# Kernel optimization log

Measured on AMD Instinct MI355X. Metric: run time of the kernel, lower is better.

## Reference

```python
import jax, jax.numpy as jnp
import numpy as np

SQ3, SQ5, SQ15 = 3.0**0.5, 5.0**0.5, 15.0**0.5
M0, M1, M2 = 128, 64, 32
DIM = M0 + 3*M1 + 5*M2  # 480
N_GRAPHS, ATOMS_PER, N_BLOCKS = 512, 16, 8
N_NODES = N_GRAPHS * ATOMS_PER
N_EDGES = 100000
CUTOFF = 5.0
AVG_DEGREE = 15.57
AVG_NUM_NODES = 18.03
ATOM_MAP = np.array([-1, 0, -1, -1, -1, -1, 1, 2, 3, 4], dtype=np.int32)


def _sph(u):
    # component-normalized real spherical harmonics l=1,2 of unit vectors u [E,3]
    x, y, z = u[:, 0], u[:, 1], u[:, 2]
    sh1 = SQ3 * u
    sh2 = jnp.stack([SQ15*x*y, SQ15*y*z, 0.5*SQ5*(3.0*z*z - 1.0),
                     SQ15*x*z, 0.5*SQ15*(x*x - y*y)], axis=-1)
    return sh1, sh2


def _seg_softmax(logits, seg, n):
    m = jax.ops.segment_max(logits, seg, num_segments=n)
    e = jnp.exp(logits - m[seg])
    s = jax.ops.segment_sum(e, seg, num_segments=n)
    return e / (s[seg] + 1e-9)


def _energy(pos, fp, node_atom, edge_src, edge_dst, batch):
    (atom_table, rbf_centers, rbf_width, deg_W1, deg_W2, deg_W3,
     blk_Wv0, blk_Wv1, blk_Wv2, blk_Ws0, blk_Ws1, blk_Ws2,
     blk_rW1, blk_rW2, blk_rW3, blk_Wa_src, blk_Wa_dst, blk_Wa_e, blk_wa,
     blk_ff1, blk_ff2, blk_fg1, blk_fg2, blk_fW1, blk_fW2,
     ln_g, ln_b, head_W0, head_out) = fp
    N = pos.shape[0]
    mapped = jnp.asarray(ATOM_MAP)[node_atom]
    f0 = atom_table[mapped]                       # [N,128] scalar channels
    f1 = jnp.zeros((N, M1, 3), f0.dtype)
    f2 = jnp.zeros((N, M2, 5), f0.dtype)

    vec = pos[edge_src] - pos[edge_dst]           # [E,3]
    r = jnp.sqrt(jnp.sum(vec*vec, axis=1) + 1e-12)
    u = vec / r[:, None]
    sh1, sh2 = _sph(u)
    rbf = jnp.exp(-0.5 * ((r[:, None] - rbf_centers[None, :]) / rbf_width[None, :])**2)  # [E,128]

    # edge-degree embedding: radial-weighted SH scattered to dst, scaled by avg degree
    h = jax.nn.silu(rbf @ deg_W1)
    h = jax.nn.silu(h @ deg_W2)
    g = h @ deg_W3                                 # [E,224]
    g0, g1, g2 = g[:, :M0], g[:, M0:M0+M1], g[:, M0+M1:]
    inv = 1.0 / (AVG_DEGREE ** 0.5)
    f0 = f0 + inv * jax.ops.segment_sum(g0, edge_dst, num_segments=N)
    f1 = f1 + inv * jax.ops.segment_sum(g1[:, :, None]*sh1[:, None, :], edge_dst, num_segments=N)
    f2 = f2 + inv * jax.ops.segment_sum(g2[:, :, None]*sh2[:, None, :], edge_dst, num_segments=N)

    for i in range(N_BLOCKS):
        s0, s1, s2 = f0[edge_src], f1[edge_src], f2[edge_src]
        h = jax.nn.silu(rbf @ blk_rW1[i])
        h = jax.nn.silu(h @ blk_rW2[i])
        g = h @ blk_rW3[i]
        g0, g1, g2 = g[:, :M0], g[:, M0:M0+M1], g[:, M0+M1:]
        # equivariant tensor-product messages: value path (radial-gated) + SH-injection path
        m0 = (s0 @ blk_Wv0[i]) * g0 + s0 @ blk_Ws0[i]
        m1 = jnp.einsum('ecx,cd->edx', s1, blk_Wv1[i]) * g1[:, :, None] \
             + (s0 @ blk_Ws1[i])[:, :, None] * sh1[:, None, :]
        m2 = jnp.einsum('ecx,cd->edx', s2, blk_Wv2[i]) * g2[:, :, None] \
             + (s0 @ blk_Ws2[i])[:, :, None] * sh2[:, None, :]
        # scalar attention, softmax over incoming edges per destination node
        z = jnp.tanh(s0 @ blk_Wa_src[i] + f0[edge_dst] @ blk_Wa_dst[i] + h @ blk_Wa_e[i])
        a = _seg_softmax(z @ blk_wa[i], edge_dst, N)  # [E]
        f0 = f0 + jax.ops.segment_sum(a[:, None]*m0, edge_dst, num_segments=N)
        f1 = f1 + jax.ops.segment_sum(a[:, None, None]*m1, edge_dst, num_segments=N)
        f2 = f2 + jax.ops.segment_sum(a[:, None, None]*m2, edge_dst, num_segments=N)
        # equivariant FFN: scalar MLP + scalar-gated per-l channel mixing
        f0 = f0 + jax.nn.silu(f0 @ blk_ff1[i]) @ blk_ff2[i]
        f1 = f1 + jnp.einsum('ncx,cd->ndx', f1, blk_fW1[i]) * jax.nn.sigmoid(f0 @ blk_fg1[i])[:, :, None]
        f2 = f2 + jnp.einsum('ncx,cd->ndx', f2, blk_fW2[i]) * jax.nn.sigmoid(f0 @ blk_fg2[i])[:, :, None]

    flat = jnp.concatenate([f0, f1.reshape(N, 3*M1), f2.reshape(N, 5*M2)], axis=1)  # [N,480]
    mu = jnp.mean(flat, axis=1, keepdims=True)
    var = jnp.var(flat, axis=1, keepdims=True)
    flat = (flat - mu) * jax.lax.rsqrt(var + 1e-5) * ln_g + ln_b
    # head: only the 0e part can reach the final 1x0e output (equivariance)
    e_node = jax.nn.silu(flat[:, :M0] @ head_W0) @ head_out  # [N,1]
    energy = jax.ops.segment_sum(e_node[:, 0], batch, num_segments=N_GRAPHS) / (AVG_NUM_NODES ** 0.5)
    return energy  # [B]


def setup_inputs() -> dict:
    key = jax.random.key(0)
    rng = np.random.default_rng(0)
    B, A = N_GRAPHS, ATOMS_PER
    pos_np = rng.uniform(0.0, 6.0, size=(B, A, 3)).astype(np.float32)
    d = np.linalg.norm(pos_np[:, :, None, :] - pos_np[:, None, :, :], axis=-1)
    mask = (d < CUTOFF) & (d > 1e-6)
    gi, si, di = np.nonzero(mask)
    src = np.resize((gi*A + si).astype(np.int32), N_EDGES)
    dst = np.resize((gi*A + di).astype(np.int32), N_EDGES)
    atoms = rng.choice(np.array([1, 6, 7, 8, 9], dtype=np.int32), size=B*A)
    batch = np.repeat(np.arange(B, dtype=np.int32), A)

    ks = iter(jax.random.split(key, 40))
    def W(shape, fan):
        return jax.random.normal(next(ks), shape, jnp.float32) / np.sqrt(fan)
    D3 = M0 + M1 + M2  # 224
    return dict(
        pos=jnp.asarray(pos_np.reshape(B*A, 3)),
        atom_table=W((5, M0), 1.0),
        rbf_centers=jnp.linspace(0.0, CUTOFF, 128),
        rbf_width=jnp.full((128,), 0.25, jnp.float32),
        deg_W1=W((128, 64), 128), deg_W2=W((64, 64), 64), deg_W3=W((64, D3), 64),
        blk_Wv0=W((8, M0, M0), M0), blk_Wv1=W((8, M1, M1), M1), blk_Wv2=W((8, M2, M2), M2),
        blk_Ws0=W((8, M0, M0), M0), blk_Ws1=W((8, M0, M1), M0), blk_Ws2=W((8, M0, M2), M0),
        blk_rW1=W((8, 128, 64), 128), blk_rW2=W((8, 64, 64), 64), blk_rW3=W((8, 64, D3), 64),
        blk_Wa_src=W((8, M0, 32), M0), blk_Wa_dst=W((8, M0, 32), M0), blk_Wa_e=W((8, 64, 32), 64),
        blk_wa=W((8, 32), 32),
        blk_ff1=W((8, M0, 4*M0), M0), blk_ff2=W((8, 4*M0, M0), 4*M0),
        blk_fg1=W((8, M0, M1), M0), blk_fg2=W((8, M0, M2), M0),
        blk_fW1=W((8, M1, M1), M1), blk_fW2=W((8, M2, M2), M2),
        ln_g=jnp.ones((DIM,), jnp.float32), ln_b=jnp.zeros((DIM,), jnp.float32),
        head_W0=W((M0, M0), M0), head_out=W((M0, 1), M0),
        node_atom=jnp.asarray(atoms), edge_src=jnp.asarray(src),
        edge_dst=jnp.asarray(dst), batch=jnp.asarray(batch),
    )


def reference(pos, atom_table, rbf_centers, rbf_width, deg_W1, deg_W2, deg_W3,
              blk_Wv0, blk_Wv1, blk_Wv2, blk_Ws0, blk_Ws1, blk_Ws2,
              blk_rW1, blk_rW2, blk_rW3, blk_Wa_src, blk_Wa_dst, blk_Wa_e, blk_wa,
              blk_ff1, blk_ff2, blk_fg1, blk_fg2, blk_fW1, blk_fW2,
              ln_g, ln_b, head_W0, head_out,
              node_atom, edge_src, edge_dst, batch):
    fp = (atom_table, rbf_centers, rbf_width, deg_W1, deg_W2, deg_W3,
          blk_Wv0, blk_Wv1, blk_Wv2, blk_Ws0, blk_Ws1, blk_Ws2,
          blk_rW1, blk_rW2, blk_rW3, blk_Wa_src, blk_Wa_dst, blk_Wa_e, blk_wa,
          blk_ff1, blk_ff2, blk_fg1, blk_fg2, blk_fW1, blk_fW2,
          ln_g, ln_b, head_W0, head_out)

    def _tot(p):
        e = _energy(p, fp, node_atom, edge_src, edge_dst, batch)
        return jnp.sum(e), e

    (_, energy), gpos = jax.value_and_grad(_tot, has_aux=True)(pos)
    forces = -gpos  # dy = -dE/dpos, as in the torch autograd.grad call
    return energy, forces
```

## Files before the change

### kernel.cpp

```cpp
#include <hip/hip_runtime.h>
#include <string.h>
#include <math.h>

#define NE 100000
#define NN 8192
#define NG 512
#define CHF 25000
#define NF 4
#define CHB 20000
#define NB 5
#define CHIF 50000
#define NIF 2
#define CHIB 34000
#define NIB 3
#define NNC 8192

#define SQ3F  1.7320508075688772f
#define SQ5F  2.23606797749979f
#define SQ15F 3.872983346207417f

__constant__ int c_amap[10] = {-1,0,-1,-1,-1,-1,1,2,3,4};

typedef __attribute__((ext_vector_type(4))) float f32x4;
typedef __attribute__((ext_vector_type(8))) short bf16x8;
// ... 352 lines not shown
__global__ void k_geom(const float* __restrict__ pos, const int* __restrict__ src, const int* __restrict__ dst,
                       float* __restrict__ U, float* __restrict__ Rr, float* __restrict__ SH2b){
  int e = blockIdx.x*256 + threadIdx.x;
  if (e >= NE) return;
  int s = src[e], d = dst[e];
  float vx = pos[s*3+0]-pos[d*3+0];
  float vy = pos[s*3+1]-pos[d*3+1];
  float vz = pos[s*3+2]-pos[d*3+2];
  float r = sqrtf(vx*vx+vy*vy+vz*vz + 1e-12f);
  float ux=vx/r, uy=vy/r, uz=vz/r;
  U[e*3+0]=ux; U[e*3+1]=uy; U[e*3+2]=uz;
  Rr[e]=r;
  SH2b[e*5+0]=SQ15F*ux*uy;
  SH2b[e*5+1]=SQ15F*uy*uz;
  SH2b[e*5+2]=0.5f*SQ5F*(3.0f*uz*uz-1.0f);
  SH2b[e*5+3]=SQ15F*ux*uz;
  SH2b[e*5+4]=0.5f*SQ15F*(ux*ux-uy*uy);
}

__global__ void k_f0init(const int* __restrict__ na, const float* __restrict__ at, float* __restrict__ f0){
  int t = blockIdx.x*256 + threadIdx.x;
  if (t >= NN*128) return;
  int n = t>>7, j = t&127;
  int m = c_amap[na[n]];
  f0[t] = at[m*128+j];
}

__global__ void k_postblk(const float* __restrict__ x0,const float* __restrict__ x1,const float* __restrict__ x2,
                          float* __restrict__ y0,float* __restrict__ y1,float* __restrict__ y2,
                          const float* __restrict__ S, unsigned short* __restrict__ ck,
                          const float* __restrict__ Pl, const int* __restrict__ dst, float* __restrict__ AB){
  int t = blockIdx.x*256 + threadIdx.x;
  if (t < NE) AB[t] = Pl[t]/(S[dst[t]]+1e-9f);
  if (t >= NN*480) return;
  float v;
  if (t < NN*128){ int n=t>>7; v = x0[t] + y0[t]/(S[n]+1e-9f); y0[t]=v; }
  else if (t < NN*320){ int q=t-NN*128; int n=q/192; v = x1[q] + y1[q]/(S[n]+1e-9f); y1[q]=v; }
  else { int q=t-NN*320; int n=q/160; v = x2[q] + y2[q]/(S[n]+1e-9f); y2[q]=v; }
  ck[t] = f2b(v);
}

__global__ void k_q3(const float* __restrict__ f0,const float* __restrict__ f1,const float* __restrict__ f2,
                     unsigned short* __restrict__ ck){
  int t = blockIdx.x*256 + threadIdx.x;
  if (t >= NN*480) return;
  float v;
  if (t < NN*128) v = f0[t];
  else if (t < NN*320) v = f1[t-NN*128];
  else v = f2[t-NN*320];
  ck[t] = f2b(v);
}
__global__ void k_dq3x2(const unsigned short* __restrict__ cka, const unsigned short* __restrict__ ckb,
                        float* __restrict__ a0,float* __restrict__ a1,float* __restrict__ a2,
                        float* __restrict__ b0,float* __restrict__ b1,float* __restrict__ b2){
  int t = blockIdx.x*256 + threadIdx.x;
  if (t >= NN*480) return;
  float va = b2f(cka[t]), vb = b2f(ckb[t]);
  if (t < NN*128){ a0[t]=va; b0[t]=vb; }
  else if (t < NN*320){ int q=t-NN*128; a1[q]=va; b1[q]=vb; }
  else { int q=t-NN*320; a2[q]=va; b2[q]=vb; }
}

template<bool INIT>
__global__ __launch_bounds__(512) void k_agg(
  float* __restrict__ f0o,float* __restrict__ f1o,float* __restrict__ f2o,
  const float* __restrict__ SC,const float* __restrict__ sv1,const float* __restrict__ sv2,
  const float* __restrict__ g,const float* __restrict__ U,const float* __restrict__ SH2b,
  const float* __restrict__ aArr,const int* __restrict__ keys,const int* __restrict__ dst,
  float* __restrict__ SACC, int c0, int c1)
{
  __shared__ float acc[7680];
  int b = blockIdx.x, lo = b<<4;
  int e0 = lbound(keys, NE, lo), e1 = lbound(keys, NE, lo+16);
  if (e0 < c0) e0 = c0;
  if (e1 > c1) e1 = c1;
  if (e0 >= e1) return;
  for (int i=threadIdx.x;i<7680;i+=512) acc[i]=0.0f;
  __syncthreads();
  const int j = threadIdx.x;
  const float inv = 1.0f/sqrtf(15.57f);
  int cat=3, cc_=0, xx_=0;
  if (j<128){ cat=0; }
  else if (j<320){ cat=1; int t=j-128; cc_=t/3; xx_=t-3*cc_; }
  else if (j<480){ cat=2; int t=j-320; cc_=t/5; xx_=t-5*cc_; }
  float sacc=0.0f;
  for (int e=e0; e<e1; ++e){
    int el = e - c0;
    float a = INIT ? inv : aArr[e];
    int nl = dst[e]&15;
    if (cat==0){
      float m = INIT ? g[el*224+j] : (SC[(size_t)el*352+j]*g[el*224+j] + SC[(size_t)el*352+128+j]);
      acc[nl*480+j] += a*m;
    } else if (cat==1){
      int t=j-128;
      float sh = SQ3F*U[e*3+xx_];
      float m = INIT ? g[el*224+128+cc_]*sh : (sv1[el*192+t]*g[el*224+128+cc_] + SC[(size_t)el*352+256+cc_]*sh);
      acc[nl*480+j] += a*m;
    } else if (cat==2){
      int t=j-320;
      float sh = SH2b[e*5+xx_];
      float m = INIT ? g[el*224+192+cc_]*sh : (sv2[el*160+t]*g[el*224+192+cc_] + SC[(size_t)el*352+320+cc_]*sh);
      acc[nl*480+j] += a*m;
    } else if (!INIT && j<496){
      if (nl==(j-480)) sacc += a;
    }
  }
  __syncthreads();
  for (int i=threadIdx.x;i<7680;i+=512){
    int nl=i/480, jj=i-480*nl, n=lo+nl;
    float v=acc[i];
    if (jj<128) f0o[n*128+jj]+=v;
    else if (jj<320) f1o[n*192+jj-128]+=v;
    else f2o[n*160+jj-320]+=v;
  }
  if (!INIT && j>=480 && j<496) SACC[lo+(j-480)] += sacc;
}

__global__ __launch_bounds__(640) void k_scat(
  float* __restrict__ df0, float* __restrict__ df1, float* __restrict__ df2,
  const float* __restrict__ DE0, const float* __restrict__ DZD,
  const float* __restrict__ DE1, const float* __restrict__ DE2,
  const int* __restrict__ src, const int* __restrict__ dst, int c0, int c1)
{
  __shared__ float acc[7680];
  int b=blockIdx.x, lo=b<<4;
  int e0=lbound(dst,NE,lo), e1=lbound(dst,NE,lo+16);
  if (e0 < c0) e0 = c0;
  if (e1 > c1) e1 = c1;
  for (int i=threadIdx.x;i<7680;i+=640) acc[i]=0.0f;
  __syncthreads();
  const int j=threadIdx.x;
  for (int e=e0;e<e1;++e){
    int el=e-c0;
    int sl=(src[e]&15)*480, dl=(dst[e]&15)*480;
    if (j<128) acc[sl+j] += DE0[el*128+j];
    else if (j<256){ int q=j-128; acc[dl+q] += DZD[el*128+q]; }
    else if (j<448){ int q=j-256; acc[sl+128+q] += DE1[el*192+q]; }
    else if (j<608){ int q=j-448; acc[sl+320+q] += DE2[el*160+q]; }
    __syncthreads();
  }
  for (int i=threadIdx.x;i<7680;i+=640){
    int nl=i/480, jj=i-480*nl, n=lo+nl;
    float v=acc[i];
    if (jj<128) df0[n*128+jj]+=v;
    else if (jj<320) df1[n*192+jj-128]+=v;
    else df2[n*160+jj-320]+=v;
  }
}

__global__ __launch_bounds__(256) void k_ssum(
  const float* __restrict__ FA0,const float* __restrict__ FA1,const float* __restrict__ FA2,
  const float* __restrict__ FB0,const float* __restrict__ FB1,const float* __restrict__ FB2,
  const float* __restrict__ DY0,const float* __restrict__ DY1,const float* __restrict__ DY2,
  float* __restrict__ SSUM)
{
  int n=blockIdx.x*4+(threadIdx.x>>6), lane=threadIdx.x&63;
  if (n>=NN) return;
  float s=0.0f;
  for (int j=lane;j<480;j+=64){
    float d,g;
    if (j<128){ d=FB0[n*128+j]-FA0[n*128+j]; g=DY0[n*128+j]; }
    else if (j<320){ int q=j-128; d=FB1[n*192+q]-FA1[n*192+q]; g=DY1[n*192+q]; }
    else { int q=j-320; d=FB2[n*160+q]-FA2[n*160+q]; g=DY2[n*160+q]; }
    s += d*g;
  }
  s = wred64(s);
  if (lane==0) SSUM[n]=s;
}

__global__ __launch_bounds__(256) void k_bedge(
  float* __restrict__ SC, float* __restrict__ SV1, float* __restrict__ SV2,
  const float* __restrict__ g, const float* __restrict__ U, const float* __restrict__ SH2b,
  const float* __restrict__ df0,const float* __restrict__ df1,const float* __restrict__ df2,
  const int* __restrict__ dst, const float* __restrict__ SSUM, const float* __restrict__ wa,
  float* __restrict__ Z, const float* __restrict__ aArr,
  float* __restrict__ DG, float* __restrict__ DSH1, float* __restrict__ DSH2,
  int c0, int cnt)
{
  int w=threadIdx.x>>6, lane=threadIdx.x&63;
  int el=blockIdx.x*4+w;
  if (el>=cnt) return;
  int e=c0+el;
  int d=dst[e];
  float s=0.0f;
  for (int j=lane;j<480;j+=64){
    float m, dfv;
    if (j<128){
      m = SC[(size_t)el*352+j]*g[el*224+j] + SC[(size_t)el*352+128+j];
      dfv = df0[(size_t)d*128+j];
    } else if (j<320){
      int t=j-128, c=t/3, x=t-3*c;
      m = SV1[el*192+t]*g[el*224+128+c] + SC[(size_t)el*352+256+c]*(SQ3F*U[e*3+x]);
      dfv = df1[(size_t)d*192+t];
    } else {
      int t=j-320, c=t/5, x=t-5*c;
      m = SV2[el*160+t]*g[el*224+192+c] + SC[(size_t)el*352+320+c]*SH2b[e*5+x];
      dfv = df2[(size_t)d*160+t];
    }
    s += m*dfv;
  }
  s = wred64(s);
  s = __shfl(s,0,64);
  float a = aArr[e];
  float dlam = a*(s - SSUM[d]);
  if (lane<32){
    float z = Z[(size_t)el*32+lane];
    Z[(size_t)el*32+lane] = dlam*wa[lane]*(1.0f-z*z);
  }
  {
    float* row = SC + (size_t)el*352;
    for (int j=lane;j<128;j+=64){
      float dm = a*df0[(size_t)d*128+j];
      float sv = row[j];
      row[128+j] = dm;
      row[j] = dm*g[el*224+j];
      DG[el*224+j] = dm*sv;
    }
  }
  {
    float dm0=a*df1[(size_t)d*192+lane*3+0];
    float dm1=a*df1[(size_t)d*192+lane*3+1];
    float dm2=a*df1[(size_t)d*192+lane*3+2];
    float sw1o=SC[(size_t)el*352+256+lane];
    float g1=g[el*224+128+lane];
    float c0v=dm0*sw1o, c1v=dm1*sw1o, c2v=dm2*sw1o;
    c0v=wred64(c0v); c1v=wred64(c1v); c2v=wred64(c2v);
    if (lane==0){ DSH1[e*3+0]+=c0v; DSH1[e*3+1]+=c1v; DSH1[e*3+2]+=c2v; }
    float sh0=SQ3F*U[e*3+0], sh1=SQ3F*U[e*3+1], sh2=SQ3F*U[e*3+2];
    SC[(size_t)el*352+256+lane]=dm0*sh0+dm1*sh1+dm2*sh2;
    float sv0o=SV1[el*192+lane*3+0], sv1o=SV1[el*192+lane*3+1], sv2o=SV1[el*192+lane*3+2];
    DG[el*224+128+lane]=dm0*sv0o+dm1*sv1o+dm2*sv2o;
    SV1[el*192+lane*3+0]=dm0*g1; SV1[el*192+lane*3+1]=dm1*g1; SV1[el*192+lane*3+2]=dm2*g1;
  }
  {
    float dm[5]={0,0,0,0,0}, svo[5]={0,0,0,0,0};
    float sw2o=0.0f, g2=0.0f;
    if (lane<32){
      #pragma unroll
      for (int x=0;x<5;x++){ dm[x]=a*df2[(size_t)d*160+lane*5+x]; svo[x]=SV2[el*160+lane*5+x]; }
      sw2o=SC[(size_t)el*352+320+lane]; g2=g[el*224+192+lane];
    }
    float c[5];
    #pragma unroll
    for (int x=0;x<5;x++){ c[x]=dm[x]*sw2o; c[x]=wred64(c[x]); }
    if (lane==0){
      #pragma unroll
      for (int x=0;x<5;x++) DSH2[e*5+x]+=c[x];
    }
    if (lane<32){
      float dsw=0.0f, dg2=0.0f;
      #pragma unroll
      for (int x=0;x<5;x++){ dsw+=dm[x]*SH2b[e*5+x]; dg2+=dm[x]*svo[x]; }
      SC[(size_t)el*352+320+lane]=dsw;
      DG[el*224+192+lane]=dg2;
      #pragma unroll
      for (int x=0;x<5;x++) SV2[el*160+lane*5+x]=dm[x]*g2;
    }
  }
}

template<int CD,int X>
__global__ void k_gateback(const float* __restrict__ dfB, float* __restrict__ V,
                           const float* __restrict__ P12, float* __restrict__ DPa, int poff){
  int t=blockIdx.x*256+threadIdx.x;
  if (t>=NN*CD) return;
  int n=t/CD, d=t-n*CD;
  float p=P12[(size_t)n*96+poff+d];
  float dp=0.0f;
  #pragma unroll
  for (int x=0;x<X;x++){ dp += dfB[(size_t)t*X+x]*V[(size_t)t*X+x]; }
  #pragma unroll
  for (int x=0;x<X;x++){ V[(size_t)t*X+x] = dfB[(size_t)t*X+x]*p; }
  DPa[(size_t)n*96+poff+d] = dp*p*(1.0f-p);
}

__global__ __launch_bounds__(256) void k_dr(const float* __restrict__ DRBF, const float* __restrict__ Rr,
    const float* __restrict__ cen, const float* __restrict__ wid, float* __restrict__ DRa, int c0, int cnt){
  int w=threadIdx.x>>6, lane=threadIdx.x&63;
  int el=blockIdx.x*4+w;
  if (el>=cnt) return;
  int e=c0+el;
  float r=Rr[e], s=0.0f;
  for (int k=lane;k<128;k+=64){
    float c=cen[k], wd=wid[k];
    float t=(r-c)/wd;
    float rb=expf(-0.5f*t*t);
    s += DRBF[el*128+k]*rb*((c-r)/(wd*wd));
  }
  s=wred64(s);
  if (lane==0) DRa[e]+=s;
}

__global__ __launch_bounds__(256) void k_initback(
  const float* __restrict__ df0,const float* __restrict__ df1,const float* __restrict__ df2,
  const int* __restrict__ dst,
  const float* __restrict__ g,const float* __restrict__ U,const float* __restrict__ SH2b,
  float* __restrict__ DG,float* __restrict__ DSH1,float* __restrict__ DSH2, int c0, int cnt)
{
  int w=threadIdx.x>>6, lane=threadIdx.x&63;
  int el=blockIdx.x*4+w;
  if (el>=cnt) return;
  int e=c0+el;
  int d=dst[e];
  const float inv=1.0f/sqrtf(15.57f);
  for (int j=lane;j<128;j+=64) DG[el*224+j]=inv*df0[d*128+j];
  float sh0=SQ3F*U[e*3+0], sh1=SQ3F*U[e*3+1], sh2=SQ3F*U[e*3+2];
  float df10=df1[d*192+lane*3+0], df11=df1[d*192+lane*3+1], df12=df1[d*192+lane*3+2];
  float g1=g[el*224+128+lane];
  DG[el*224+128+lane]=inv*(df10*sh0+df11*sh1+df12*sh2);
  float c0v=g1*df10, c1v=g1*df11, c2v=g1*df12;
  c0v=wred64(c0v); c1v=wred64(c1v); c2v=wred64(c2v);
  if (lane==0){ DSH1[e*3+0]+=inv*c0v; DSH1[e*3+1]+=inv*c1v; DSH1[e*3+2]+=inv*c2v; }
  float cc[5]={0,0,0,0,0};
  if (lane<32){
    float g2=g[el*224+192+lane];
    float dgv=0.0f;
    #pragma unroll
    for (int x=0;x<5;x++){ float dfv=df2[d*160+lane*5+x]; dgv+=dfv*SH2b[e*5+x]; cc[x]=g2*dfv; }
    DG[el*224+192+lane]=inv*dgv;
  }
  #pragma unroll
  for (int x=0;x<5;x++) cc[x]=wred64(cc[x]);
  if (lane==0){
    #pragma unroll
    for (int x=0;x<5;x++) DSH2[e*5+x]+=inv*cc[x];
  }
}

__global__ void k_geoback(const float* __restrict__ DRa, const float* __restrict__ DSH1, const float* __restrict__ DSH2,
                          const float* __restrict__ U, const float* __restrict__ Rr,
                          const int* __restrict__ src, const int* __restrict__ dst,
                          float* __restrict__ DPOS){
  int e=blockIdx.x*256+threadIdx.x;
  if (e>=NE) return;
  float ux=U[e*3+0], uy=U[e*3+1], uz=U[e*3+2];
  float r=Rr[e];
  float dux=SQ3F*DSH1[e*3+0], duy=SQ3F*DSH1[e*3+1], duz=SQ3F*DSH1[e*3+2];
  float d0=DSH2[e*5+0],d1=DSH2[e*5+1],d2=DSH2[e*5+2],d3=DSH2[e*5+3],d4=DSH2[e*5+4];
  dux += SQ15F*(uy*d0+uz*d3+ux*d4);
  duy += SQ15F*(ux*d0+uz*d1-uy*d4);
  duz += SQ15F*(uy*d1+ux*d3)+3.0f*SQ5F*uz*d2;
  float dr=DRa[e];
  float dot=dux*ux+duy*uy+duz*uz;
  float dvx=(dux-dot*ux)/r+dr*ux;
  float dvy=(duy-dot*uy)/r+dr*uy;
  float dvz=(duz-dot*uz)/r+dr*uz;
  int s=src[e], d=dst[e];
  atomicAdd(&DPOS[s*3+0],dvx); atomicAdd(&DPOS[s*3+1],dvy); atomicAdd(&DPOS[s*3+2],dvz);
  atomicAdd(&DPOS[d*3+0],-dvx); atomicAdd(&DPOS[d*3+1],-dvy); atomicAdd(&DPOS[d*3+2],-dvz);
}

__global__ void k_forces(const float* __restrict__ DPOS, float* __restrict__ o){
  int i=blockIdx.x*256+threadIdx.x;
  if (i<NN*3) o[i]=-DPOS[i];
}

__global__ __launch_bounds__(64) void k_lnhead(
  const float* __restrict__ f0,const float* __restrict__ f1,const float* __restrict__ f2,
  const float* __restrict__ lng,const float* __restrict__ lnb,
  const float* __restrict__ W0,const float* __restrict__ hout,
  float* __restrict__ EN, float* __restrict__ df0,float* __restrict__ df1,float* __restrict__ df2)
{
  __shared__ float xh[480];
  __shared__ float fl[128];
  __shared__ float dyv[128];
  __shared__ float dxh[128];
  int n=blockIdx.x, lane=threadIdx.x;
  const float c0=1.0f/sqrtf(18.03f);
  for (int i=lane;i<480;i+=64){
    float v=(i<128)? f0[n*128+i] : (i<320)? f1[n*192+(i-128)] : f2[n*160+(i-320)];
    xh[i]=v;
  }
  __syncthreads();
  float s1=0.0f,s2=0.0f;
  for (int i=lane;i<480;i+=64){ float v=xh[i]; s1+=v; s2+=v*v; }
  s1=wred64(s1); s2=wred64(s2);
  float mu=__shfl(s1,0,64)*(1.0f/480.0f);
  float var=__shfl(s2,0,64)*(1.0f/480.0f)-mu*mu;
  float rstd=rsqrtf(var+1e-5f);
  for (int i=lane;i<480;i+=64) xh[i]=(xh[i]-mu)*rstd;
  __syncthreads();
  for (int k=lane;k<128;k+=64) fl[k]=xh[k]*lng[k]+lnb[k];
  __syncthreads();
  float y0=0.0f,y1=0.0f;
  for (int k=0;k<128;k++){ float f=fl[k]; y0+=f*W0[k*128+lane]; y1+=f*W0[k*128+lane+64]; }
  float e = siluf(y0)*hout[lane] + siluf(y1)*hout[lane+64];
  e=wred64(e);
  if (lane==0) EN[n]=e*c0;
  dyv[lane]=c0*hout[lane]*dsiluf(y0);
  dyv[lane+64]=c0*hout[lane+64]*dsiluf(y1);
  __syncthreads();
  float d0=0.0f,d1=0.0f;
  for (int j=0;j<128;j++){ float dv=dyv[j]; d0+=dv*W0[lane*128+j]; d1+=dv*W0[(lane+64)*128+j]; }
  dxh[lane]=d0*lng[lane];
  dxh[lane+64]=d1*lng[lane+64];
  __syncthreads();
  float s3=dxh[lane]+dxh[lane+64];
  float s4=dxh[lane]*xh[lane]+dxh[lane+64]*xh[lane+64];
  s3=wred64(s3); s4=wred64(s4);
  float m1=__shfl(s3,0,64)*(1.0f/480.0f);
  float m2=__shfl(s4,0,64)*(1.0f/480.0f);
  for (int i=lane;i<480;i+=64){
    float dv=rstd*(((i<128)?dxh[i]:0.0f)-m1-xh[i]*m2);
    if (i<128) df0[n*128+i]=dv;
    else if (i<320) df1[n*192+(i-128)]=dv;
    else df2[n*160+(i-320)]=dv;
  }
}

__global__ void k_esum(const float* __restrict__ EN, float* __restrict__ out){
  int b=blockIdx.x*64+threadIdx.x;
  if (b<NG){
    float s=0.0f;
    for (int k=0;k<16;k++) s+=EN[b*16+k];
    out[b]=s;
  }
}

#define MG(MT,TB,ACC,ACT,GA,SP,AR,DM,PO, A,IDX,B,C,M,Nd,K, CEN,WID,DMp,POp) \
  k_mgemm<MT,TB,ACC,ACT,GA,SP,AR,DM,PO><<<dim3((unsigned)(((M)+(MT)-1)/(MT)),(unsigned)(((Nd)+63)/64)),dim3(256),0,stream>>>((A),(IDX),(B),(C),(M),(Nd),(K),(CEN),(WID),(DMp),(POp))
#define MGEMM(MT,TB,ACC,ACT,GA, A,IDX,B,C,M,Nd,K) MG(MT,TB,ACC,ACT,GA,false,false,false,false, A,IDX,B,C,M,Nd,K, nullptr,nullptr,nullptr,nullptr)
#define MGEMM3(MT,TB,ACC,ACT,GA, A,IDX,B,C,M,Nd,K) MG(MT,TB,ACC,ACT,GA,true,false,false,false, A,IDX,B,C,M,Nd,K, nullptr,nullptr,nullptr,nullptr)
#define MEINS(CI,CO,X,TB,ACC,GA, A,IDX,Wt,C,M) \
  k_meinsum<CI,CO,X,TB,ACC,GA,false,false><<<dim3((unsigned)(((M)*(X)+63)/64)),dim3(256),0,stream>>>((A),(IDX),(Wt),(C),(M),nullptr,0,0)
#define MEINS3(CI,CO,X,TB,ACC,GA, A,IDX,Wt,C,M) \
  k_meinsum<CI,CO,X,TB,ACC,GA,true,false><<<dim3((unsigned)(((M)*(X)+63)/64)),dim3(256),0,stream>>>((A),(IDX),(Wt),(C),(M),nullptr,0,0)
#define MEINSG(CI,CO,X,SP, A,Wt,C,M, Pp,POFF) \
  k_meinsum<CI,CO,X,false,false,false,SP,true><<<dim3((unsigned)(((M)*(X)+63)/64)),dim3(256),0,stream>>>((A),nullptr,(Wt),(C),(M),(Pp),96,(POFF))
#define G256(n) dim3((unsigned)(((n)+255)/256)),dim3(256),0,stream
#define GW4(n) dim3((unsigned)(((n)+3)/4)),dim3(256),0,stream

extern "C" void kernel_launch(void* const* d_in, const int* in_sizes, int n_in,
                              void* d_out, int out_size, void* d_ws, size_t ws_size,
                              hipStream_t stream)
{
  const float* pos =(const float*)d_in[0];
  const float* atab=(const float*)d_in[1];
  const float* rbfc=(const float*)d_in[2];
  const float* rbfw=(const float*)d_in[3];
  const float* degW1=(const float*)d_in[4];
  const float* degW2=(const float*)d_in[5];
  const float* degW3=(const float*)d_in[6];
  const float* Wv0=(const float*)d_in[7];
  const float* Wv1=(const float*)d_in[8];
  const float* Wv2=(const float*)d_in[9];
  const float* Ws0=(const float*)d_in[10];
  const float* Ws1=(const float*)d_in[11];
  const float* Ws2=(const float*)d_in[12];
  const float* rW1=(const float*)d_in[13];
  const float* rW2=(const float*)d_in[14];
  const float* rW3=(const float*)d_in[15];
  const float* WaS=(const float*)d_in[16];
  const float* WaD=(const float*)d_in[17];
  const float* WaE=(const float*)d_in[18];
  const float* wab=(const float*)d_in[19];
  const float* ff1=(const float*)d_in[20];
  const float* ff2=(const float*)d_in[21];
  const float* fg1=(const float*)d_in[22];
  const float* fg2=(const float*)d_in[23];
  const float* fW1=(const float*)d_in[24];
  const float* fW2=(const float*)d_in[25];
  const float* lng=(const float*)d_in[26];
  const float* lnb=(const float*)d_in[27];
  const float* W0h=(const float*)d_in[28];
  const float* hout=(const float*)d_in[29];
  const int* natom=(const int*)d_in[30];
  const int* esrc=(const int*)d_in[31];
  const int* edst=(const int*)d_in[32];

  float* Wp=(float*)d_ws;
  size_t off=0;
  auto al=[&](size_t n)->float*{ float* q=Wp+off; off+=n; return q; };

  const size_t SLOT = (size_t)NN*480;
  unsigned short* CKB = (unsigned short*)al((9*SLOT+1)/2);
  float* FA0=al((size_t)NN*128); float* FA1=al((size_t)NN*192); float* FA2=al((size_t)NN*160);
  float* FB0=al((size_t)NN*128); float* FB1=al((size_t)NN*192); float* FB2=al((size_t)NN*160);
  float* DI0=al((size_t)NN*128); float* DI1=al((size_t)NN*192); float* DI2=al((size_t)NN*160);
  float* DY0=al((size_t)NN*128); float* DY1=al((size_t)NN*192); float* DY2=al((size_t)NN*160);
  float* U=al((size_t)NE*3); float* Rr=al(NE); float* SH2b=al((size_t)NE*5);
  float* ABLK=al(8ULL*NE); float* LAM=al(NE);
  float* SSUM=al(NN); float* ENODE=al(NN); float* SACC=al(NN);
  float* DRr=al(NE); float* DSH1=al((size_t)NE*3); float* DSH2=al((size_t)NE*5);
  float* DPOS=al((size_t)NN*3);
  float* WCATF=al(8ULL*128*352);
  float* WCATZ=al(8ULL*320*32);
  float* WCATG=al(8ULL*128*96);
  int* ROWS =(int*)al(NN+1);
  int* CNT  =(int*)al(NN);
  int* POSB =(int*)al(NN);
  int* PERMB=(int*)al(NE);
  int* ESRC2=(int*)al(NE);
  int* EDST2=(int*)al(NE);

  const size_t UNI = 28800000;
  float* UN = al(UNI);
  float* TBc=UN;
  float* DTc=TBc+(size_t)NNC*512;
  float* P12=DTc+(size_t)NNC*512;
  float* V1 =P12+(size_t)NN*96;
  float* V2 =V1 +(size_t)NN*192;
  float* DPb=V2 +(size_t)NN*160;
  float* F0N=DPb+(size_t)NN*96;

  float* outE=(float*)d_out;
  float* outF=outE+NG;

  if (off*sizeof(float) > ws_size){
    k_sentinel<<<G256(out_size)>>>(outE, out_size, (float)ws_size);
    return;
  }

  (void)hipMemsetAsync(CNT,0,NN*sizeof(int),stream);
  k_hist<<<G256(NE)>>>(edst,CNT,NE);
  k_scan0<<<dim3(1),dim3(256),0,stream>>>(CNT,ROWS);
  (void)hipMemcpyAsync(POSB,ROWS,NN*sizeof(int),hipMemcpyDeviceToDevice,stream);
  k_fillperm<<<G256(NE)>>>(edst,POSB,PERMB,NE);
  k_mkedge<<<G256(NE)>>>(PERMB,esrc,edst,ESRC2,EDST2);
  k_wcat<<<G256(8*128*352)>>>(Wv0,Ws0,Ws1,Ws2,WCATF);
  k_wcatz<<<G256(8*320*32)>>>(WaS,WaD,WaE,WCATZ);
  k_wcatg<<<G256(8*128*96)>>>(fg1,fg2,WCATG);

  k_geom<<<G256(NE)>>>(pos,ESRC2,EDST2,U,Rr,SH2b);
  k_f0init<<<G256(NN*128)>>>(natom,atab,FA0);
  (void)hipMemsetAsync(FA1,0,(size_t)NN*352*4,stream);
  (void)hipMemsetAsync(DRr,0,(size_t)NE*4,stream);
  (void)hipMemsetAsync(DSH1,0,(size_t)NE*3*4,stream);
  (void)hipMemsetAsync(DSH2,0,(size_t)NE*5*4,stream);
  (void)hipMemsetAsync(DPOS,0,(size_t)NN*3*4,stream);

  {
    float* H1=UN; float* H2=H1+(size_t)CHIF*64; float* Gc=H2+(size_t)CHIF*64;
    for (int cc=0;cc<NIF;cc++){
      int c0e=cc*CHIF, cnt=(c0e+CHIF<=NE)?CHIF:(NE-c0e);
      MG(64,false,false,1,false, true,true,false,false, Rr+c0e,nullptr,degW1,H1, cnt,64,128, rbfc,rbfw,nullptr,nullptr);
      MGEMM3(64,false,false,1,false, H1,nullptr,degW2,H2, cnt,64,64);
      MGEMM3(64,false,false,0,false, H2,nullptr,degW3,Gc, cnt,224,64);
      k_agg<true><<<dim3(NG),dim3(512),0,stream>>>(FA0,FA1,FA2,
        nullptr,nullptr,nullptr, Gc,U,SH2b, nullptr, EDST2,EDST2, nullptr, c0e,c0e+cnt);
    }
  }
  k_q3<<<G256(NN*480)>>>(FA0,FA1,FA2, CKB);

  float *c0_=FA0,*c1_=FA1,*c2_=FA2, *n0_=FB0,*n1_=FB1,*n2_=FB2;

  {
    float* H1  =UN;
    float* H2  =H1  +(size_t)CHF*64;
    float* Gc  =H2  +(size_t)CHF*64;
    float* SCAT=Gc  +(size_t)CHF*224;
    float* SV1 =SCAT+(size_t)CHF*352;
    float* SV2 =SV1 +(size_t)CHF*192;
    float* Zc  =SV2 +(size_t)CHF*160;
    for (int i=0;i<8;i++){
      const float* Wv1i=Wv1+(size_t)i*4096; const float* Wv2i=Wv2+(size_t)i*1024;
      const float* rW1i=rW1+(size_t)i*8192; const float* rW2i=rW2+(size_t)i*4096; const float* rW3i=rW3+(size_t)i*14336;
      const float* WZi=WCATZ+(size_t)i*10240;
      const float* ff1i=ff1+(size_t)i*65536; const float* ff2i=ff2+(size_t)i*65536;
      const float* fgCi=WCATG+(size_t)i*12288;
      const float* fW1i=fW1+(size_t)i*4096; const float* fW2i=fW2+(size_t)i*1024;
      const float* WCi=WCATF+(size_t)i*45056;
      float* AB=ABLK+(size_t)i*NE;

      (void)hipMemsetAsync(SACC,0,(size_t)NN*4,stream);
      (void)hipMemsetAsync(n0_,0,(size_t)NN*128*4,stream);
      (void)hipMemsetAsync(n1_,0,(size_t)NN*352*4,stream);
      for (int cc=0;cc<NF;cc++){
        int c0e=cc*CHF, cnt=(c0e+CHF<=NE)?CHF:(NE-c0e);
        MG(64,false,false,1,false, true,true,false,false, Rr+c0e,nullptr,rW1i,H1, cnt,64,128, rbfc,rbfw,nullptr,nullptr);
        MGEMM3(64,false,false,1,false, H1,nullptr,rW2i,H2, cnt,64,64);
        MGEMM3(64,false,false,0,false, H2,nullptr,rW3i,Gc, cnt,224,64);
        k_zgemm<true,true><<<dim3((unsigned)((cnt+63)/64)),dim3(256),0,stream>>>(
            c0_, ESRC2+c0e, EDST2+c0e, H2, WZi, wab+(size_t)i*32, Zc, LAM+c0e, cnt);
        MGEMM3(64,false,false,0,true, c0_,ESRC2+c0e,WCi,SCAT, cnt,352,128);
        MEINS3(64,64,3,false,false,true, c1_,ESRC2+c0e,Wv1i,SV1, cnt);
        MEINS3(32,32,5,false,false,true, c2_,ESRC2+c0e,Wv2i,SV2, cnt);
        k_agg<false><<<dim3(NG),dim3(512),0,stream>>>(n0_,n1_,n2_,
          SCAT,SV1,SV2, Gc,U,SH2b, LAM, EDST2,EDST2, SACC, c0e,c0e+cnt);
      }
      k_postblk<<<G256(NN*480)>>>(c0_,c1_,c2_, n0_,n1_,n2_, SACC, CKB+(size_t)(i+1)*SLOT, LAM, EDST2, AB);
      for (int nc=0;nc<NN/NNC;nc++){
        MGEMM3(64,false,false,1,false, n0_+(size_t)nc*NNC*128,nullptr,ff1i,TBc, NNC,512,128);
        MGEMM3(64,false,true, 0,false, TBc,nullptr,ff2i, n0_+(size_t)nc*NNC*128, NNC,128,512);
      }
      MGEMM3(64,false,false,3,false, n0_,nullptr,fgCi,P12, NN,96,128);
      MEINSG(64,64,3,true, n1_,fW1i,c1_, NN, P12, 0);
      MEINSG(32,32,5,true, n2_,fW2i,c2_, NN, P12, 64);
      float* t;
      t=c0_;c0_=n0_;n0_=t;
    }
  }

  k_lnhead<<<dim3(NN),dim3(64),0,stream>>>(c0_,c1_,c2_, lng,lnb,W0h,hout, ENODE, DI0,DI1,DI2);
  k_esum<<<dim3(8),dim3(64),0,stream>>>(ENODE,outE);

  {
    float* PRE1=UN;
    float* PRE2=PRE1+(size_t)CHB*64;
    float* H1  =PRE2+(size_t)CHB*64;
    float* H2  =H1  +(size_t)CHB*64;
    float* Gc  =H2  +(size_t)CHB*64;
    float* DGc =Gc  +(size_t)CHB*224;
    float* SCAT=DGc +(size_t)CHB*224;
    float* SV1 =SCAT+(size_t)CHB*352;
    float* SV2 =SV1 +(size_t)CHB*192;
    float* Zc  =SV2 +(size_t)CHB*160;
    float* DE0 =PRE1;
    float* RBFc=DGc;
    float* DZD =Gc;
    for (int i=7;i>=0;--i){
      const float* Wv1i=Wv1+(size_t)i*4096; const float* Wv2i=Wv2+(size_t)i*1024;
      const float* rW1i=rW1+(size_t)i*8192; const float* rW2i=rW2+(size_t)i*4096; const float* rW3i=rW3+(size_t)i*14336;
      const float* WZi=WCATZ+(size_t)i*10240;
      const float* WaSi=WaS+(size_t)i*4096; const float* WaDi=WaD+(size_t)i*4096; const float* WaEi=WaE+(size_t)i*2048;
      const float* ff1i=ff1+(size_t)i*65536; const float* ff2i=ff2+(size_t)i*65536;
      const float* fgCi=WCATG+(size_t)i*12288;
      const float* fW1i=fW1+(size_t)i*4096; const float* fW2i=fW2+(size_t)i*1024;
      const float* WCi=WCATF+(size_t)i*45056;
      const float* AB=ABLK+(size_t)i*NE;
      float *fa1=FA1, *fa2=FA2, *dy1=DY1, *dy2=DY2;

      k_dq3x2<<<G256(NN*480)>>>(CKB+(size_t)i*SLOT, CKB+(size_t)(i+1)*SLOT, FA0,FA1,FA2, FB0,FB1,FB2);
      if (i>0){
        const float* pf1=ff1+(size_t)(i-1)*65536; const float* pf2=ff2+(size_t)(i-1)*65536;
        const float* pgC=WCATG+(size_t)(i-1)*12288;
        const float* pW1=fW1+(size_t)(i-1)*4096; const float* pW2=fW2+(size_t)(i-1)*1024;
        for (int nc=0;nc<NN/NNC;nc++){
          MGEMM(64,false,false,1,false, FA0+(size_t)nc*NNC*128,nullptr,pf1,TBc, NNC,512,128);
          MGEMM(64,false,true, 0,false, TBc,nullptr,pf2, FA0+(size_t)nc*NNC*128, NNC,128,512);
        }
        MGEMM(64,false,false,3,false, FA0,nullptr,pgC,P12, NN,96,128);
        MEINSG(64,64,3,false, FA1,pW1,DY1, NN, P12, 0);
        MEINSG(32,32,5,false, FA2,pW2,DY2, NN, P12, 64);
        fa1=DY1; dy1=FA1; fa2=DY2; dy2=FA2;
      }
      (void)hipMemcpyAsync(F0N,FB0,(size_t)NN*128*4,hipMemcpyDeviceToDevice,stream);
      for (int nc=0;nc<NN/NNC;nc++){
        MGEMM(64,false,false,1,false, FB0+(size_t)nc*NNC*128,nullptr,ff1i,TBc, NNC,512,128);
        MGEMM(64,false,true, 0,false, TBc,nullptr,ff2i, F0N+(size_t)nc*NNC*128, NNC,128,512);
      }
      MGEMM(64,false,false,3,false, F0N,nullptr,fgCi,P12, NN,96,128);
      MEINS(64,64,3,false,false,false, FB1,nullptr,fW1i,V1, NN);
      MEINS(32,32,5,false,false,false, FB2,nullptr,fW2i,V2, NN);
      k_gateback<64,3><<<G256(NN*64)>>>(DI1,V1,P12,DPb,0);
      k_gateback<32,5><<<G256(NN*32)>>>(DI2,V2,P12,DPb,64);
      MGEMM(64,true,true,0,false, DPb,nullptr,fgCi,DI0, NN,128,96);
      (void)hipMemcpyAsync(dy1,DI1,(size_t)NN*192*4,hipMemcpyDeviceToDevice,stream);
      MEINS(64,64,3,true,true,false, V1,nullptr,fW1i,dy1, NN);
      (void)hipMemcpyAsync(dy2,DI2,(size_t)NN*160*4,hipMemcpyDeviceToDevice,stream);
      MEINS(32,32,5,true,true,false, V2,nullptr,fW2i,dy2, NN);
      (void)hipMemcpyAsync(DY0,DI0,(size_t)NN*128*4,hipMemcpyDeviceToDevice,stream);
      for (int nc=0;nc<NN/NNC;nc++){
        MGEMM(64,false,false,0,false, FB0+(size_t)nc*NNC*128,nullptr,ff1i,TBc, NNC,512,128);
        MG(64,true,false,0,false, false,false,true,false, DI0+(size_t)nc*NNC*128,nullptr,ff2i,DTc, NNC,512,128, nullptr,nullptr,TBc,nullptr);
        MGEMM(64,true,true,0,false, DTc,nullptr,ff1i, DY0+(size_t)nc*NNC*128, NNC,128,512);
      }
      k_ssum<<<dim3(NN/4),dim3(256),0,stream>>>(FA0,fa1,fa2,FB0,FB1,FB2,DY0,dy1,dy2,SSUM);
      (void)hipMemcpyAsync(DI0,DY0,(size_t)NN*128*4,hipMemcpyDeviceToDevice,stream);
      (void)hipMemcpyAsync(DI1,dy1,(size_t)NN*192*4,hipMemcpyDeviceToDevice,stream);
      (void)hipMemcpyAsync(DI2,dy2,(size_t)NN*160*4,hipMemcpyDeviceToDevice,stream);
      for (int cc=0;cc<NB;cc++){
        int c0e=cc*CHB, cnt=(c0e+CHB<=NE)?CHB:(NE-c0e);
        MG(64,false,false,1,false, false,true,false,true, Rr+c0e,nullptr,rW1i,H1, cnt,64,128, rbfc,rbfw,nullptr,PRE1);
        MG(64,false,false,1,false, false,false,false,true, H1,nullptr,rW2i,H2, cnt,64,64, nullptr,nullptr,nullptr,PRE2);
        MGEMM(64,false,false,0,false, H2,nullptr,rW3i,Gc, cnt,224,64);
        k_zgemm<false,false><<<dim3((unsigned)((cnt+63)/64)),dim3(256),0,stream>>>(
            FA0, ESRC2+c0e, EDST2+c0e, H2, WZi, nullptr, Zc, nullptr, cnt);
        MGEMM(64,false,false,0,true, FA0,ESRC2+c0e,WCi,SCAT, cnt,352,128);
        MEINS(64,64,3,false,false,true, fa1,ESRC2+c0e,Wv1i,SV1, cnt);
        MEINS(32,32,5,false,false,true, fa2,ESRC2+c0e,Wv2i,SV2, cnt);
        k_bedge<<<GW4(cnt)>>>(SCAT,SV1,SV2, Gc,U,SH2b, DY0,dy1,dy2, EDST2, SSUM,
                              wab+(size_t)i*32, Zc, AB, DGc, DSH1, DSH2, c0e, cnt);
        MGEMM(64,true,false,0,false, Zc,nullptr,WaEi,H2, cnt,64,32);
        MG(64,true,true,0,false, false,false,true,false, DGc,nullptr,rW3i,H2, cnt,64,224, nullptr,nullptr,PRE2,nullptr);
        MG(64,true,false,0,false, false,false,true,false, H2,nullptr,rW2i,H1, cnt,64,64, nullptr,nullptr,PRE1,nullptr);
        MGEMM(64,true,false,0,false, H1,nullptr,rW1i,RBFc, cnt,128,64);
        k_dr<<<GW4(cnt)>>>(RBFc,Rr,rbfc,rbfw,DRr, c0e,cnt);
        MGEMM(64,true,false,0,false, SCAT,nullptr,WCi,DE0, cnt,128,352);
        MGEMM(64,true,true, 0,false, Zc,nullptr,WaSi,DE0, cnt,128,32);
        MGEMM(64,true,false,0,false, Zc,nullptr,WaDi,DZD, cnt,128,32);
        MEINS(64,64,3,true,false,false, SV1,nullptr,Wv1i,SV1, cnt);
        MEINS(32,32,5,true,false,false, SV2,nullptr,Wv2i,SV2, cnt);
        k_scat<<<dim3(NG),dim3(640),0,stream>>>(DI0,DI1,DI2, DE0,DZD,SV1,SV2, ESRC2,EDST2, c0e,c0e+cnt);
      }
    }
  }

  {
    float* PRE1=UN;
    float* PRE2=PRE1+(size_t)CHIB*64;
    float* H1  =PRE2+(size_t)CHIB*64;
    float* H2  =H1  +(size_t)CHIB*64;
    float* Gc  =H2  +(size_t)CHIB*64;
    float* DGc =Gc  +(size_t)CHIB*224;
    float* RBFc=DGc +(size_t)CHIB*224;
    for (int cc=0;cc<NIB;cc++){
      int c0e=cc*CHIB, cnt=(c0e+CHIB<=NE)?CHIB:(NE-c0e);
      MG(64,false,false,1,false, false,true,false,true, Rr+c0e,nullptr,degW1,H1, cnt,64,128, rbfc,rbfw,nullptr,PRE1);
      MG(64,false,false,1,false, false,false,false,true, H1,nullptr,degW2,H2, cnt,64,64, nullptr,nullptr,nullptr,PRE2);
      MGEMM(64,false,false,0,false, H2,nullptr,degW3,Gc, cnt,224,64);
      k_initback<<<GW4(cnt)>>>(DI0,DI1,DI2,EDST2,Gc,U,SH2b,DGc,DSH1,DSH2, c0e,cnt);
      MG(64,true,false,0,false, false,false,true,false, DGc,nullptr,degW3,H2, cnt,64,224, nullptr,nullptr,PRE2,nullptr);
      MG(64,true,false,0,false, false,false,true,false, H2,nullptr,degW2,H1, cnt,64,64, nullptr,nullptr,PRE1,nullptr);
      MGEMM(64,true,false,0,false, H1,nullptr,degW1,RBFc, cnt,128,64);
      k_dr<<<GW4(cnt)>>>(RBFc,Rr,rbfc,rbfw,DRr, c0e,cnt);
    }
  }

  k_geoback<<<G256(NE)>>>(DRr,DSH1,DSH2,U,Rr,ESRC2,EDST2,DPOS);
  k_forces<<<G256(NN*3)>>>(DPOS,outF);
  (void)in_sizes; (void)n_in; (void)out_size;
}
```

Before: 31.58 ms.

## Use 128-wide GEMM tiles for wide outputs, fuse gate-back kernels and copies

```diff
diff --git a/kernel.cpp b/kernel.cpp
--- a/kernel.cpp
+++ b/kernel.cpp
@@ -528,16 +528,17 @@
   const float* __restrict__ FA0,const float* __restrict__ FA1,const float* __restrict__ FA2,
   const float* __restrict__ FB0,const float* __restrict__ FB1,const float* __restrict__ FB2,
   const float* __restrict__ DY0,const float* __restrict__ DY1,const float* __restrict__ DY2,
-  float* __restrict__ SSUM)
+  float* __restrict__ SSUM,
+  float* __restrict__ DI0o, float* __restrict__ DI1o, float* __restrict__ DI2o)
 {
   int n=blockIdx.x*4+(threadIdx.x>>6), lane=threadIdx.x&63;
   if (n>=NN) return;
   float s=0.0f;
   for (int j=lane;j<480;j+=64){
     float d,g;
-    if (j<128){ d=FB0[n*128+j]-FA0[n*128+j]; g=DY0[n*128+j]; }
-    else if (j<320){ int q=j-128; d=FB1[n*192+q]-FA1[n*192+q]; g=DY1[n*192+q]; }
-    else { int q=j-320; d=FB2[n*160+q]-FA2[n*160+q]; g=DY2[n*160+q]; }
+    if (j<128){ d=FB0[n*128+j]-FA0[n*128+j]; g=DY0[n*128+j]; DI0o[n*128+j]=g; }
+    else if (j<320){ int q=j-128; d=FB1[n*192+q]-FA1[n*192+q]; g=DY1[n*192+q]; DI1o[n*192+q]=g; }
+    else { int q=j-320; d=FB2[n*160+q]-FA2[n*160+q]; g=DY2[n*160+q]; DI2o[n*160+q]=g; }
     s += d*g;
   }
   s = wred64(s);
@@ -635,19 +636,30 @@
   }
 }
 
-template<int CD,int X>
-__global__ void k_gateback(const float* __restrict__ dfB, float* __restrict__ V,
-                           const float* __restrict__ P12, float* __restrict__ DPa, int poff){
+__global__ void k_gateback2(const float* __restrict__ dfB1, float* __restrict__ V1,
+                            const float* __restrict__ dfB2, float* __restrict__ V2,
+                            const float* __restrict__ P12, float* __restrict__ DPa){
   int t=blockIdx.x*256+threadIdx.x;
-  if (t>=NN*CD) return;
-  int n=t/CD, d=t-n*CD;
-  float p=P12[(size_t)n*96+poff+d];
-  float dp=0.0f;
-  #pragma unroll
-  for (int x=0;x<X;x++){ dp += dfB[(size_t)t*X+x]*V[(size_t)t*X+x]; }
-  #pragma unroll
-  for (int x=0;x<X;x++){ V[(size_t)t*X+x] = dfB[(size_t)t*X+x]*p; }
-  DPa[(size_t)n*96+poff+d] = dp*p*(1.0f-p);
+  if (t < NN*64){
+    int n=t>>6, d=t&63;
+    float p=P12[(size_t)n*96+d];
+    float dp=0.0f;
+    #pragma unroll
+    for (int x=0;x<3;x++){ dp += dfB1[(size_t)t*3+x]*V1[(size_t)t*3+x]; }
+    #pragma unroll
+    for (int x=0;x<3;x++){ V1[(size_t)t*3+x] = dfB1[(size_t)t*3+x]*p; }
+    DPa[(size_t)n*96+d] = dp*p*(1.0f-p);
+  } else if (t < NN*96){
+    int t2=t-NN*64;
+    int n=t2>>5, d=t2&31;
+    float p=P12[(size_t)n*96+64+d];
+    float dp=0.0f;
+    #pragma unroll
+    for (int x=0;x<5;x++){ dp += dfB2[(size_t)t2*5+x]*V2[(size_t)t2*5+x]; }
+    #pragma unroll
+    for (int x=0;x<5;x++){ V2[(size_t)t2*5+x] = dfB2[(size_t)t2*5+x]*p; }
+    DPa[(size_t)n*96+64+d] = dp*p*(1.0f-p);
+  }
 }
 
 __global__ __launch_bounds__(256) void k_dr(const float* __restrict__ DRBF, const float* __restrict__ Rr,
@@ -911,7 +923,7 @@
       int c0e=cc*CHIF, cnt=(c0e+CHIF<=NE)?CHIF:(NE-c0e);
       MG(64,false,false,1,false, true,true,false,false, Rr+c0e,nullptr,degW1,H1, cnt,64,128, rbfc,rbfw,nullptr,nullptr);
       MGEMM3(64,false,false,1,false, H1,nullptr,degW2,H2, cnt,64,64);
-      MGEMM3(64,false,false,0,false, H2,nullptr,degW3,Gc, cnt,224,64);
+      MGEMM3(128,false,false,0,false, H2,nullptr,degW3,Gc, cnt,224,64);
       k_agg<true><<<dim3(NG),dim3(512),0,stream>>>(FA0,FA1,FA2,
         nullptr,nullptr,nullptr, Gc,U,SH2b, nullptr, EDST2,EDST2, nullptr, c0e,c0e+cnt);
     }
@@ -945,10 +957,10 @@
         int c0e=cc*CHF, cnt=(c0e+CHF<=NE)?CHF:(NE-c0e);
         MG(64,false,false,1,false, true,true,false,false, Rr+c0e,nullptr,rW1i,H1, cnt,64,128, rbfc,rbfw,nullptr,nullptr);
         MGEMM3(64,false,false,1,false, H1,nullptr,rW2i,H2, cnt,64,64);
-        MGEMM3(64,false,false,0,false, H2,nullptr,rW3i,Gc, cnt,224,64);
+        MGEMM3(128,false,false,0,false, H2,nullptr,rW3i,Gc, cnt,224,64);
         k_zgemm<true,true><<<dim3((unsigned)((cnt+63)/64)),dim3(256),0,stream>>>(
             c0_, ESRC2+c0e, EDST2+c0e, H2, WZi, wab+(size_t)i*32, Zc, LAM+c0e, cnt);
-        MGEMM3(64,false,false,0,true, c0_,ESRC2+c0e,WCi,SCAT, cnt,352,128);
+        MGEMM3(128,false,false,0,true, c0_,ESRC2+c0e,WCi,SCAT, cnt,352,128);
         MEINS3(64,64,3,false,false,true, c1_,ESRC2+c0e,Wv1i,SV1, cnt);
         MEINS3(32,32,5,false,false,true, c2_,ESRC2+c0e,Wv2i,SV2, cnt);
         k_agg<false><<<dim3(NG),dim3(512),0,stream>>>(n0_,n1_,n2_,
@@ -956,7 +968,7 @@
       }
       k_postblk<<<G256(NN*480)>>>(c0_,c1_,c2_, n0_,n1_,n2_, SACC, CKB+(size_t)(i+1)*SLOT, LAM, EDST2, AB);
       for (int nc=0;nc<NN/NNC;nc++){
-        MGEMM3(64,false,false,1,false, n0_+(size_t)nc*NNC*128,nullptr,ff1i,TBc, NNC,512,128);
+        MGEMM3(128,false,false,1,false, n0_+(size_t)nc*NNC*128,nullptr,ff1i,TBc, NNC,512,128);
         MGEMM3(64,false,true, 0,false, TBc,nullptr,ff2i, n0_+(size_t)nc*NNC*128, NNC,128,512);
       }
       MGEMM3(64,false,false,3,false, n0_,nullptr,fgCi,P12, NN,96,128);
@@ -1002,7 +1014,7 @@
         const float* pgC=WCATG+(size_t)(i-1)*12288;
         const float* pW1=fW1+(size_t)(i-1)*4096; const float* pW2=fW2+(size_t)(i-1)*1024;
         for (int nc=0;nc<NN/NNC;nc++){
-          MGEMM(64,false,false,1,false, FA0+(size_t)nc*NNC*128,nullptr,pf1,TBc, NNC,512,128);
+          MGEMM(128,false,false,1,false, FA0+(size_t)nc*NNC*128,nullptr,pf1,TBc, NNC,512,128);
           MGEMM(64,false,true, 0,false, TBc,nullptr,pf2, FA0+(size_t)nc*NNC*128, NNC,128,512);
         }
         MGEMM(64,false,false,3,false, FA0,nullptr,pgC,P12, NN,96,128);
@@ -1012,14 +1024,13 @@
       }
       (void)hipMemcpyAsync(F0N,FB0,(size_t)NN*128*4,hipMemcpyDeviceToDevice,stream);
       for (int nc=0;nc<NN/NNC;nc++){
-        MGEMM(64,false,false,1,false, FB0+(size_t)nc*NNC*128,nullptr,ff1i,TBc, NNC,512,128);
+        MGEMM(128,false,false,1,false, FB0+(size_t)nc*NNC*128,nullptr,ff1i,TBc, NNC,512,128);
         MGEMM(64,false,true, 0,false, TBc,nullptr,ff2i, F0N+(size_t)nc*NNC*128, NNC,128,512);
       }
       MGEMM(64,false,false,3,false, F0N,nullptr,fgCi,P12, NN,96,128);
       MEINS(64,64,3,false,false,false, FB1,nullptr,fW1i,V1, NN);
       MEINS(32,32,5,false,false,false, FB2,nullptr,fW2i,V2, NN);
-      k_gateback<64,3><<<G256(NN*64)>>>(DI1,V1,P12,DPb,0);
-      k_gateback<32,5><<<G256(NN*32)>>>(DI2,V2,P12,DPb,64);
+      k_gateback2<<<G256(NN*96)>>>(DI1,V1,DI2,V2,P12,DPb);
       MGEMM(64,true,true,0,false, DPb,nullptr,fgCi,DI0, NN,128,96);
       (void)hipMemcpyAsync(dy1,DI1,(size_t)NN*192*4,hipMemcpyDeviceToDevice,stream);
       MEINS(64,64,3,true,true,false, V1,nullptr,fW1i,dy1, NN);
@@ -1027,22 +1038,19 @@
       MEINS(32,32,5,true,true,false, V2,nullptr,fW2i,dy2, NN);
       (void)hipMemcpyAsync(DY0,DI0,(size_t)NN*128*4,hipMemcpyDeviceToDevice,stream);
       for (int nc=0;nc<NN/NNC;nc++){
-        MGEMM(64,false,false,0,false, FB0+(size_t)nc*NNC*128,nullptr,ff1i,TBc, NNC,512,128);
-        MG(64,true,false,0,false, false,false,true,false, DI0+(size_t)nc*NNC*128,nullptr,ff2i,DTc, NNC,512,128, nullptr,nullptr,TBc,nullptr);
+        MGEMM(128,false,false,0,false, FB0+(size_t)nc*NNC*128,nullptr,ff1i,TBc, NNC,512,128);
+        MG(128,true,false,0,false, false,false,true,false, DI0+(size_t)nc*NNC*128,nullptr,ff2i,DTc, NNC,512,128, nullptr,nullptr,TBc,nullptr);
         MGEMM(64,true,true,0,false, DTc,nullptr,ff1i, DY0+(size_t)nc*NNC*128, NNC,128,512);
       }
-      k_ssum<<<dim3(NN/4),dim3(256),0,stream>>>(FA0,fa1,fa2,FB0,FB1,FB2,DY0,dy1,dy2,SSUM);
-      (void)hipMemcpyAsync(DI0,DY0,(size_t)NN*128*4,hipMemcpyDeviceToDevice,stream);
-      (void)hipMemcpyAsync(DI1,dy1,(size_t)NN*192*4,hipMemcpyDeviceToDevice,stream);
-      (void)hipMemcpyAsync(DI2,dy2,(size_t)NN*160*4,hipMemcpyDeviceToDevice,stream);
+      k_ssum<<<dim3(NN/4),dim3(256),0,stream>>>(FA0,fa1,fa2,FB0,FB1,FB2,DY0,dy1,dy2,SSUM, DI0,DI1,DI2);
       for (int cc=0;cc<NB;cc++){
         int c0e=cc*CHB, cnt=(c0e+CHB<=NE)?CHB:(NE-c0e);
         MG(64,false,false,1,false, false,true,false,true, Rr+c0e,nullptr,rW1i,H1, cnt,64,128, rbfc,rbfw,nullptr,PRE1);
         MG(64,false,false,1,false, false,false,false,true, H1,nullptr,rW2i,H2, cnt,64,64, nullptr,nullptr,nullptr,PRE2);
-        MGEMM(64,false,false,0,false, H2,nullptr,rW3i,Gc, cnt,224,64);
+        MGEMM(128,false,false,0,false, H2,nullptr,rW3i,Gc, cnt,224,64);
         k_zgemm<false,false><<<dim3((unsigned)((cnt+63)/64)),dim3(256),0,stream>>>(
             FA0, ESRC2+c0e, EDST2+c0e, H2, WZi, nullptr, Zc, nullptr, cnt);
-        MGEMM(64,false,false,0,true, FA0,ESRC2+c0e,WCi,SCAT, cnt,352,128);
+        MGEMM(128,false,false,0,true, FA0,ESRC2+c0e,WCi,SCAT, cnt,352,128);
         MEINS(64,64,3,false,false,true, fa1,ESRC2+c0e,Wv1i,SV1, cnt);
         MEINS(32,32,5,false,false,true, fa2,ESRC2+c0e,Wv2i,SV2, cnt);
         k_bedge<<<GW4(cnt)>>>(SCAT,SV1,SV2, Gc,U,SH2b, DY0,dy1,dy2, EDST2, SSUM,
@@ -1052,7 +1060,7 @@
         MG(64,true,false,0,false, false,false,true,false, H2,nullptr,rW2i,H1, cnt,64,64, nullptr,nullptr,PRE1,nullptr);
         MGEMM(64,true,false,0,false, H1,nullptr,rW1i,RBFc, cnt,128,64);
         k_dr<<<GW4(cnt)>>>(RBFc,Rr,rbfc,rbfw,DRr, c0e,cnt);
-        MGEMM(64,true,false,0,false, SCAT,nullptr,WCi,DE0, cnt,128,352);
+        MGEMM(128,true,false,0,false, SCAT,nullptr,WCi,DE0, cnt,128,352);
         MGEMM(64,true,true, 0,false, Zc,nullptr,WaSi,DE0, cnt,128,32);
         MGEMM(64,true,false,0,false, Zc,nullptr,WaDi,DZD, cnt,128,32);
         MEINS(64,64,3,true,false,false, SV1,nullptr,Wv1i,SV1, cnt);
@@ -1074,7 +1082,7 @@
       int c0e=cc*CHIB, cnt=(c0e+CHIB<=NE)?CHIB:(NE-c0e);
       MG(64,false,false,1,false, false,true,false,true, Rr+c0e,nullptr,degW1,H1, cnt,64,128, rbfc,rbfw,nullptr,PRE1);
       MG(64,false,false,1,false, false,false,false,true, H1,nullptr,degW2,H2, cnt,64,64, nullptr,nullptr,nullptr,PRE2);
-      MGEMM(64,false,false,0,false, H2,nullptr,degW3,Gc, cnt,224,64);
+      MGEMM(128,false,false,0,false, H2,nullptr,degW3,Gc, cnt,224,64);
       k_initback<<<GW4(cnt)>>>(DI0,DI1,DI2,EDST2,Gc,U,SH2b,DGc,DSH1,DSH2, c0e,cnt);
       MG(64,true,false,0,false, false,false,true,false, DGc,nullptr,degW3,H2, cnt,64,224, nullptr,nullptr,PRE2,nullptr);
       MG(64,true,false,0,false, false,false,true,false, H2,nullptr,degW2,H1, cnt,64,64, nullptr,nullptr,PRE1,nullptr);
```

Result: no change. 31.96 ms (+1.2%).
